# Optimization experiments

Hardware: AMD Instinct MI355X
Metric: run time of the kernel (lower is better)

The kernel has to match this reference:

```python
import jax, jax.numpy as jnp
import numpy as np

EMBED = 1024
HEADS = 16
HDIM = 64
OUT = 1024
SCALE = HDIM ** (-0.5)


def setup_inputs() -> dict:
    key = jax.random.key(0)
    ks = jax.random.split(key, 12)
    B, L = 4, 1024
    k = jax.random.normal(ks[0], (B, L, EMBED), dtype=jnp.float32)
    q = jax.random.normal(ks[1], (B, L, EMBED), dtype=jnp.float32)
    v = jax.random.normal(ks[2], (B, L, EMBED), dtype=jnp.float32)
    # Linear params stored as [in, out]; scaled like torch default init
    lim = EMBED ** (-0.5)
    Wq = jax.random.uniform(ks[3], (EMBED, HEADS * HDIM), jnp.float32, -lim, lim)
    bq = jax.random.uniform(ks[4], (HEADS * HDIM,), jnp.float32, -lim, lim)
    Wk = jax.random.uniform(ks[5], (EMBED, HEADS * HDIM), jnp.float32, -lim, lim)
    Wv = jax.random.uniform(ks[6], (EMBED, HEADS * HDIM), jnp.float32, -lim, lim)
    limp = (HEADS * HDIM) ** (-0.5)
    Wp = jax.random.uniform(ks[7], (HEADS * HDIM, OUT), jnp.float32, -limp, limp)
    bp = jax.random.uniform(ks[8], (OUT,), jnp.float32, -limp, limp)
    attn_w = jax.random.uniform(ks[9], (2 * HDIM,), jnp.float32, -SCALE, SCALE)
    gamma = jnp.ones((OUT,), jnp.float32)
    beta = jnp.zeros((OUT,), jnp.float32)
    return {"k": k, "q": q, "v": v, "Wq": Wq, "bq": bq, "Wk": Wk, "Wv": Wv,
            "Wp": Wp, "bp": bp, "attn_w": attn_w, "gamma": gamma, "beta": beta}


def reference(k, q, v, Wq, bq, Wk, Wv, Wp, bp, attn_w, gamma, beta):
    B, Lq = q.shape[0], q.shape[1]
    Lk = k.shape[1]
    # QKV projections -> (b, len, heads, hdim)
    qh = (q @ Wq + bq).reshape(B, Lq, HEADS, HDIM)
    kh = (k @ Wk).reshape(B, Lk, HEADS, HDIM)
    vh = (v @ Wv).reshape(B, Lk, HEADS, HDIM)
    # mlp score: tanh(cat(q_i, k_j) . w) == tanh(q_i.w1 + k_j.w2); avoids
    # materializing the (b, q, k, n, 2d) padded tensor from the original.
    w1, w2 = attn_w[:HDIM], attn_w[HDIM:]
    sq = jnp.einsum('bind,d->bin', qh, w1)  # (b, q_len, heads)
    sk = jnp.einsum('bjnd,d->bjn', kh, w2)  # (b, k_len, heads)
    attn = jnp.tanh(sq[:, :, None, :] + sk[:, None, :, :])  # (b, i, j, n)
    attn = jax.nn.softmax(attn, axis=2)  # softmax over k_len (dim=2)
    out = jnp.einsum('bijn,bjnd->bind', attn, vh).reshape(B, Lq, HEADS * HDIM)
    out = out @ Wp + bp
    # LayerNorm eps=1e-6 (dropout is identity at p=0)
    mean = jnp.mean(out, axis=-1, keepdims=True)
    var = jnp.var(out, axis=-1, keepdims=True)
    out = (out - mean) / jnp.sqrt(var + 1e-6) * gamma + beta
    return out
```

## Files before the change

kernel.cpp:

```cpp
#include <hip/hip_runtime.h>
#include <math.h>

#define SEQ   1024
#define EMB   1024
#define MN    16

typedef _Float16 f16;
typedef __attribute__((ext_vector_type(4))) _Float16 f16x4;
typedef __attribute__((ext_vector_type(8))) _Float16 f16x8;
typedef __attribute__((ext_vector_type(4))) float f32x4;

__global__ __launch_bounds__(256) void prep_kernel(
    const float* __restrict__ Wq, const float* __restrict__ Wk,
    const float* __restrict__ bq, const float* __restrict__ aw,
    const float* __restrict__ v, const float* __restrict__ Wv,
    float* __restrict__ uq, float* __restrict__ uk,
    float* __restrict__ cq, float* __restrict__ Wn,
    f16* __restrict__ vTh, f16* __restrict__ WvTh)
{
  __shared__ float tile[64][65];
  const int t = blockIdx.x, tid = threadIdx.x;
  if (t < 128) {
    int idx = t*256 + tid;
    bool isQ = idx < 16384;
    int li = isQ ? idx : idx - 16384;
    int e = li >> 4, n = li & 15;
    const float* W = isQ ? Wq : Wk;
    const float* w = isQ ? aw : aw + 64;
    const float* wp = &W[(size_t)e*EMB + n*64];
    float s = 0.f;
    #pragma unroll 16
    for (int d = 0; d < 64; ++d) s = fmaf(wp[d], w[d], s);
    (isQ ? uq : uk)[li] = s;
  } else if (t < 1408) {
    int tt = t - 128;
    int z = tt >> 8;
    int ty = (tt >> 4) & 15, tx = tt & 15;
    int r0 = ty*64, c0 = tx*64;
    const float* src = (z < 4) ? &v[(size_t)(z*SEQ + r0)*EMB + c0]
                               : &Wv[(size_t)r0*EMB + c0];
    int rr = tid >> 4, c4 = (tid & 15)*4;
    #pragma unroll
    for (int i = 0; i < 4; ++i) {
      int row = rr + i*16;
      float4 wv = *reinterpret_cast<const float4*>(&src[(size_t)row*EMB + c4]);
      tile[row][c4] = wv.x; tile[row][c4+1] = wv.y;
      tile[row][c4+2] = wv.z; tile[row][c4+3] = wv.w;
    }
    __syncthreads();
    #pragma unroll
    for (int i = 0; i < 4; ++i) {
      int cc = rr + i*16;
      f16x4 hh;
      #pragma unroll
      for (int jj = 0; jj < 4; ++jj) hh[jj] = (f16)tile[c4+jj][cc];
      size_t o = (z < 4) ? ((size_t)(z*EMB + c0 + cc))*SEQ + r0 + c4
                         : ((size_t)(c0 + cc))*EMB + r0 + c4;
      *reinterpret_cast<f16x4*>(&((z < 4) ? vTh : WvTh)[o]) = hh;
    }
  } else if (t == 1408) {
    if (tid < 16) {
      float s = 0.f;
      for (int d = 0; d < 64; ++d) s = fmaf(bq[tid*64+d], aw[d], s);
      cq[tid] = s;
    }
  } else {
    for (int u = tid; u < 1024; u += 256) Wn[u] = 0.f;
  }
}

__global__ __launch_bounds__(256) void sqsk2_kernel(
    const float* __restrict__ q, const float* __restrict__ k,
    const float* __restrict__ uq, const float* __restrict__ uk,
    const float* __restrict__ cq, float* __restrict__ sq, float* __restrict__ sk)
{
  __shared__ float rowbuf[8][EMB];
  __shared__ float part[16][8][17];
  int bid = blockIdx.x;
  bool isQ = bid < 512;
  int row0 = (isQ ? bid : bid - 512)*8;
  const float* X = isQ ? q : k;
  const float* U = isQ ? uq : uk;
  int tid = threadIdx.x;
  #pragma unroll
  for (int p = 0; p < 8; ++p) {
    int fi = p*256 + tid;
    int r = fi >> 8, c4 = (fi & 255)*4;
    *reinterpret_cast<float4*>(&rowbuf[r][c4]) =
        *reinterpret_cast<const float4*>(&X[(size_t)(row0+r)*EMB + c4]);
  }
  __syncthreads();
  int n = tid & 15, ch = tid >> 4;
  float acc[8] = {0,0,0,0,0,0,0,0};
  #pragma unroll 4
  for (int e0 = 0; e0 < 64; ++e0) {
    int e = ch*64 + e0;
    float u = U[e*16 + n];
    #pragma unroll
    for (int r = 0; r < 8; ++r) acc[r] = fmaf(rowbuf[r][e], u, acc[r]);
  }
  #pragma unroll
  for (int r = 0; r < 8; ++r) part[ch][r][n] = acc[r];
  __syncthreads();
  if (tid < 128) {
    int r = tid >> 4, nn = tid & 15;
    float s = isQ ? cq[nn] : 0.f;
    #pragma unroll
    for (int c = 0; c < 16; ++c) s += part[c][r][nn];
    (isQ ? sq : sk)[(size_t)(row0+r)*16 + nn] = s;
  }
}

__global__ __launch_bounds__(256) void wmatn_kernel(
    const float* __restrict__ sq, const float* __restrict__ sk,
    f16* __restrict__ wh, float* __restrict__ nodes, float* __restrict__ Wn)
{
  __shared__ float smn[256], smx[256];
  __shared__ float nodesh[MN], Wnl[MN];
  const int qd = blockIdx.x, n = blockIdx.y, b = blockIdx.z;
  const int tid = threadIdx.x;
  float mn = 1e30f, mx = -1e30f;
  #pragma unroll
  for (int s = 0; s < 4; ++s) {
    float vv = sq[((size_t)(b*SEQ + tid + s*256))*16 + n];
    mn = fminf(mn, vv); mx = fmaxf(mx, vv);
  }
  smn[tid] = mn; smx[tid] = mx;
  __syncthreads();
  for (int off = 128; off > 0; off >>= 1) {
    if (tid < off) { smn[tid] = fminf(smn[tid], smn[tid+off]);
                     smx[tid] = fmaxf(smx[tid], smx[tid+off]); }
    __syncthreads();
  }
  if (tid < MN) {
    float c = 0.5f*(smn[0]+smx[0]);
    float r = fmaxf(0.5f*(smx[0]-smn[0]), 1e-4f);
    float nv = c + r*cosf(tid*(3.14159265358979323f/(MN-1)));
    nodesh[tid] = nv;
    Wnl[tid] = 0.f;
    if (qd == 0) nodes[(b*16+n)*MN + tid] = nv;
  }
  __syncthreads();
  const int j = qd*256 + tid;
  const float skv = sk[((size_t)(b*SEQ + j))*16 + n];
  const int lane = tid & 63;
  #pragma unroll 4
  for (int m = 0; m < MN; ++m) {
    float s = nodesh[m] + skv;
    float e2 = __expf(2.f*s);
    float th = 1.f - 2.f/(e2+1.f);
    float w = __expf(th);
    wh[(size_t)(b*256 + n*MN + m)*1024 + j] = (f16)w;
    float ws = w;
    #pragma unroll
    for (int off = 32; off > 0; off >>= 1) ws += __shfl_xor(ws, off);
    if (lane == 0) atomicAdd(&Wnl[m], ws);
  }
  __syncthreads();
  if (tid < MN) atomicAdd(&Wn[(b*16+n)*MN + tid], Wnl[tid]);
}

__global__ __launch_bounds__(256) void g1c_kernel(
    const f16* __restrict__ wh, const f16* __restrict__ vTh,
    f16* __restrict__ Ph,
    const float* __restrict__ sq, const float* __restrict__ nodes,
    const float* __restrict__ Wn, f16* __restrict__ csh, f16* __restrict__ csl)
{
  __shared__ __align__(16) char SMEM[16384];
  const int t = blockIdx.x, tid = threadIdx.x;
  if (t < 256) {
    int swz = (t & 7)*32 + (t >> 3);
    int bx = swz & 15, by = swz >> 4;
    int z = by >> 2;
    int grow = by*64, bcol = bx*64;
    int wid = tid >> 6, lane = tid & 63;
    int wm = wid >> 1, wn = wid & 1;
    int asel = lane >> 4, l15 = lane & 15;
    const f16* Bz = vTh + (size_t)z*EMB*SEQ;
    char* lds = SMEM;
    f32x4 acc[2][2];
    #pragma unroll
    for (int i = 0; i < 2; ++i)
      #pragma unroll
      for (int jx = 0; jx < 2; ++jx)
        acc[i][jx] = (f32x4){0.f,0.f,0.f,0.f};
    for (int kt = 0; kt < 16; ++kt) {
      const int k0 = kt*64;
      __syncthreads();
      #pragma unroll
      for (int r = 0; r < 4; ++r) {
        int ci = ((r & 1) << 8) + tid;
        int row = ci >> 3, kc = ci & 7;
        int kcg = kc ^ (row & 7);
        const f16* base = (r < 2) ? wh : Bz;
        size_t roff = (r < 2) ? (size_t)(grow + row) : (size_t)(bcol + row);
        const char* src = (const char*)(base + roff*1024 + k0 + kcg*8);
        char* dst = lds + (r*256 + wid*64)*16;
        __builtin_amdgcn_global_load_lds(
            (const __attribute__((address_space(1))) unsigned int*)src,
            (__attribute__((address_space(3))) unsigned int*)dst, 16, 0, 0);
      }
      __syncthreads();
      #pragma unroll
      for (int kk = 0; kk < 2; ++kk) {
        f16x8 afh[2], bfh[2];
        #pragma unroll
        for (int mf = 0; mf < 2; ++mf) {
          int row = wm*32 + mf*16 + l15;
          int kcx = (kk*4 + asel) ^ (row & 7);
          afh[mf] = *reinterpret_cast<const f16x8*>(lds + row*128 + kcx*16);
        }
        #pragma unroll
        for (int nf = 0; nf < 2; ++nf) {
          int col = wn*32 + nf*16 + l15;
          int kcx = (kk*4 + asel) ^ (col & 7);
          bfh[nf] = *reinterpret_cast<const f16x8*>(lds + 8192 + col*128 + kcx*16);
        }
        #pragma unroll
        for (int mf = 0; mf < 2; ++mf)
          #pragma unroll
          for (int nf = 0; nf < 2; ++nf)
            acc[mf][nf] = __builtin_amdgcn_mfma_f32_16x16x32_f16(afh[mf], bfh[nf], acc[mf][nf], 0, 0, 0);
      }
    }
    const int crow0 = grow + wm*32 + asel*4;
    const int ccol0 = bcol + wn*32 + l15;
    #pragma unroll
    for (int nf = 0; nf < 2; ++nf)
      #pragma unroll
      for (int mf = 0; mf < 2; ++mf)
        #pragma unroll
        for (int jx = 0; jx < 4; ++jx)
          Ph[(size_t)(crow0 + mf*16 + jx)*1024 + ccol0 + nf*16] = (f16)acc[mf][nf][jx];
  } else {
    int tc = t - 256;
    int ic = tc & 63, b = tc >> 6;
    float (*nsh)[MN] = (float(*)[MN])SMEM;
    float (*wsh)[MN] = ((float(*)[MN])SMEM) + 16;
    {
      int nn = tid >> 4, mm = tid & 15;
      nsh[nn][mm] = nodes[(b*16+nn)*MN + mm];
      wsh[nn][mm] = Wn[(b*16+nn)*MN + mm];
    }
    __syncthreads();
    int il = tid >> 4, n = tid & 15;
    int i = ic*16 + il;
    float s = sq[((size_t)(b*SEQ + i))*16 + n];
    float lam[MN];
    float den = 0.f;
    int ex = -1;
    #pragma unroll
    for (int m = 0; m < MN; ++m) {
      float diff = s - nsh[n][m];
      float wb = ((m == 0) | (m == MN-1)) ? 0.5f : 1.0f;
      wb = (m & 1) ? -wb : wb;
      if (diff == 0.f) ex = m;
      lam[m] = wb / diff;
      den = fmaf(lam[m], wsh[n][m], den);
    }
    float rden = 1024.f / den;
    f16* hp = &csh[((size_t)(b*SEQ + i))*256 + n*MN];
    f16* lp = &csl[((size_t)(b*SEQ + i))*256 + n*MN];
    #pragma unroll
    for (int m8 = 0; m8 < 2; ++m8) {
      f16x8 hv, lv;
      #pragma unroll
      for (int jj = 0; jj < 8; ++jj) {
        int m = m8*8 + jj;
        float c = (ex >= 0) ? ((m == ex) ? 1024.f/wsh[n][ex] : 0.f) : lam[m]*rden;
        f16 h = (f16)c;
        hv[jj] = h; lv[jj] = (f16)(c - (float)h);
      }
      *reinterpret_cast<f16x8*>(&hp[m8*8]) = hv;
      *reinterpret_cast<f16x8*>(&lp[m8*8]) = lv;
    }
  }
}

__global__ __launch_bounds__(256) void ghprep_kernel(
    const f16* __restrict__ Ph, const f16* __restrict__ WvTh,
    const float* __restrict__ Wp, f16* __restrict__ Hsh, f16* __restrict__ Hsl)
{
  __shared__ float Gsh[MN][64];
  const int oc = blockIdx.x, n = blockIdx.y, b = blockIdx.z;
  const int bn = b*16 + n;
  const int tid = threadIdx.x;
  const int w = tid >> 6, lane = tid & 63;
  const int l15 = lane & 15, asel = lane >> 4;
  f32x4 acc = (f32x4){0.f,0.f,0.f,0.f};
  #pragma unroll 4
  for (int ks = 0; ks < 32; ++ks) {
    size_t bo = ((size_t)(n*64 + w*16 + l15))*1024 + ks*32 + asel*8;
    f16x8 bh = *reinterpret_cast<const f16x8*>(&WvTh[bo]);
    size_t ao = ((size_t)(bn*MN + l15))*1024 + ks*32 + asel*8;
    f16x8 ah = *reinterpret_cast<const f16x8*>(&Ph[ao]);
    acc = __builtin_amdgcn_mfma_f32_16x16x32_f16(ah, bh, acc, 0, 0, 0);
  }
  #pragma unroll
  for (int jx = 0; jx < 4; ++jx)
    Gsh[asel*4 + jx][w*16 + l15] = acc[jx];
  __syncthreads();
  const int o = oc*256 + tid;
  float a2[MN];
  #pragma unroll
  for (int m = 0; m < MN; ++m) a2[m] = 0.f;
  for (int d = 0; d < 64; ++d) {
    float wp = Wp[(size_t)(n*64 + d)*1024 + o];
    #pragma unroll
    for (int m = 0; m < MN; ++m) a2[m] = fmaf(wp, Gsh[m][d], a2[m]);
  }
  f16 hbuf[MN], lbuf[MN];
  #pragma unroll
  for (int m = 0; m < MN; ++m) {
    float vv = a2[m] * (1.f/1024.f);
    f16 h = (f16)vv;
    hbuf[m] = h; lbuf[m] = (f16)(vv - (float)h);
  }
  size_t base = ((size_t)(b*1024 + o))*256 + n*MN;
  #pragma unroll
  for (int m8 = 0; m8 < 2; ++m8) {
    *reinterpret_cast<f16x8*>(&Hsh[base + m8*8]) = *reinterpret_cast<f16x8*>(&hbuf[m8*8]);
    *reinterpret_cast<f16x8*>(&Hsl[base + m8*8]) = *reinterpret_cast<f16x8*>(&lbuf[m8*8]);
  }
}

__global__ __launch_bounds__(256) void gemm2_k(
    const f16* __restrict__ Ah, const f16* __restrict__ Al,
    const f16* __restrict__ Bh, const f16* __restrict__ Bl,
    const float* __restrict__ bias, float* __restrict__ Cf)
{
  __shared__ __align__(16) char lds[49152];
  const int tid = threadIdx.x;
  const int wid = tid >> 6, lane = tid & 63;
  int flat = (blockIdx.z * 8 + blockIdx.y) * 16 + blockIdx.x;
  int swz = (flat & 7) * 64 + (flat >> 3);
  const int bx = swz & 15;
  const int t2 = swz >> 4;
  const int by = t2 & 7, z = t2 >> 3;
  const int brow = by * 128;
  const int bcol = bx * 64;
  const int wm = wid >> 1, wn = wid & 1;
  const int asel = lane >> 4, l15 = lane & 15;
  const int K = 256, N = 1024, MZ = 1024;
  const f16* Az_h = Ah + (size_t)z*MZ*K;
  const f16* Az_l = Al + (size_t)z*MZ*K;
  const f16* Bz_h = Bh + (size_t)z*N*K;
  const f16* Bz_l = Bl + (size_t)z*N*K;

  f32x4 acc[4][2];
  #pragma unroll
  for (int i = 0; i < 4; ++i)
    #pragma unroll
    for (int jx = 0; jx < 2; ++jx)
      acc[i][jx] = (f32x4){0.f, 0.f, 0.f, 0.f};

  for (int t = 0; t < 4; ++t) {
    const int k0 = t * 64;
    __syncthreads();
    #pragma unroll
    for (int r = 0; r < 12; ++r) {
      const char* src;
      if (r < 8) {
        int ci = ((r & 3) << 8) + tid;
        int row = ci >> 3, kc = ci & 7;
        int kcg = kc ^ (row & 7);
        const f16* base = (r < 4) ? Az_h : Az_l;
        src = (const char*)(base + (size_t)(brow + row) * K + k0 + kcg * 8);
      } else {
        int ci = ((r & 1) << 8) + tid;
        int col = ci >> 3, kc = ci & 7;
        int kcg = kc ^ (col & 7);
        const f16* base = (r < 10) ? Bz_h : Bz_l;
        src = (const char*)(base + (size_t)(bcol + col) * K + k0 + kcg * 8);
      }
      char* dst = lds + (r * 256 + wid * 64) * 16;
      __builtin_amdgcn_global_load_lds(
          (const __attribute__((address_space(1))) unsigned int*)src,
          (__attribute__((address_space(3))) unsigned int*)dst, 16, 0, 0);
    }
    __syncthreads();
    #pragma unroll
    for (int kk = 0; kk < 2; ++kk) {
      f16x8 afh[4], afl[4], bfh[2], bfl[2];
      #pragma unroll
      for (int mf = 0; mf < 4; ++mf) {
        int row = wm * 64 + mf * 16 + l15;
        int kcx = (kk * 4 + asel) ^ (row & 7);
        int off = row * 128 + kcx * 16;
        afh[mf] = *reinterpret_cast<const f16x8*>(lds + off);
        afl[mf] = *reinterpret_cast<const f16x8*>(lds + 16384 + off);
      }
      #pragma unroll
      for (int nf = 0; nf < 2; ++nf) {
        int col = wn * 32 + nf * 16 + l15;
        int kcx = (kk * 4 + asel) ^ (col & 7);
        int off = col * 128 + kcx * 16;
        bfh[nf] = *reinterpret_cast<const f16x8*>(lds + 32768 + off);
        bfl[nf] = *reinterpret_cast<const f16x8*>(lds + 40960 + off);
      }
      #pragma unroll
      for (int mf = 0; mf < 4; ++mf)
        #pragma unroll
        for (int nf = 0; nf < 2; ++nf) {
          acc[mf][nf] = __builtin_amdgcn_mfma_f32_16x16x32_f16(afh[mf], bfh[nf], acc[mf][nf], 0, 0, 0);
          acc[mf][nf] = __builtin_amdgcn_mfma_f32_16x16x32_f16(afh[mf], bfl[nf], acc[mf][nf], 0, 0, 0);
          acc[mf][nf] = __builtin_amdgcn_mfma_f32_16x16x32_f16(afl[mf], bfh[nf], acc[mf][nf], 0, 0, 0);
        }
    }
  }
  const int crow0 = z*MZ + brow + wm * 64 + asel * 4;
  const int ccol0 = bcol + wn * 32 + l15;
  #pragma unroll
  for (int nf = 0; nf < 2; ++nf) {
    float bv = bias[ccol0 + nf * 16];
    #pragma unroll
    for (int mf = 0; mf < 4; ++mf)
      #pragma unroll
      for (int jx = 0; jx < 4; ++jx)
        Cf[(size_t)(crow0 + mf*16 + jx) * N + ccol0 + nf*16] = acc[mf][nf][jx] + bv;
  }
}

__global__ __launch_bounds__(256) void ln_kernel(
    float* __restrict__ out, const float* __restrict__ gamma,
    const float* __restrict__ beta)
{
  const int t = blockIdx.x, tid = threadIdx.x;
  int wid = tid >> 6, lane = tid & 63;
  int row = t*4 + wid;
  float4 x[4];
  float sum = 0.f, ssq = 0.f;
  #pragma unroll
  for (int p = 0; p < 4; ++p) {
    x[p] = *reinterpret_cast<float4*>(&out[(size_t)row*1024 + (p*64 + lane)*4]);
    sum += x[p].x + x[p].y + x[p].z + x[p].w;
    ssq += x[p].x*x[p].x + x[p].y*x[p].y + x[p].z*x[p].z + x[p].w*x[p].w;
  }
  #pragma unroll
  for (int off = 32; off > 0; off >>= 1) {
    sum += __shfl_xor(sum, off);
    ssq += __shfl_xor(ssq, off);
  }
  float mean = sum * (1.f/1024.f);
  float var  = ssq * (1.f/1024.f) - mean*mean;
  float inv  = 1.0f / sqrtf(var + 1e-6f);
  #pragma unroll
  for (int p = 0; p < 4; ++p) {
    float4 gv = *reinterpret_cast<const float4*>(&gamma[(p*64 + lane)*4]);
    float4 bv = *reinterpret_cast<const float4*>(&beta[(p*64 + lane)*4]);
    float4 y;
    y.x = (x[p].x - mean)*inv*gv.x + bv.x;
    y.y = (x[p].y - mean)*inv*gv.y + bv.y;
    y.z = (x[p].z - mean)*inv*gv.z + bv.z;
    y.w = (x[p].w - mean)*inv*gv.w + bv.w;
    *reinterpret_cast<float4*>(&out[(size_t)row*1024 + (p*64 + lane)*4]) = y;
  }
}

extern "C" void kernel_launch(void* const* d_in, const int* in_sizes, int n_in,
                              void* d_out, int out_size, void* d_ws, size_t ws_size,
                              hipStream_t stream)
{
  const float* k   = (const float*)d_in[0];
  const float* q   = (const float*)d_in[1];
  const float* v   = (const float*)d_in[2];
  const float* Wq  = (const float*)d_in[3];
  const float* bq  = (const float*)d_in[4];
  const float* Wk  = (const float*)d_in[5];
  const float* Wv  = (const float*)d_in[6];
  const float* Wp  = (const float*)d_in[7];
  const float* bp  = (const float*)d_in[8];
  const float* aw  = (const float*)d_in[9];
  const float* gamma = (const float*)d_in[10];
  const float* beta  = (const float*)d_in[11];
  float* out = (float*)d_out;

  float* ws    = (float*)d_ws;
  float* uq    = ws;
  float* uk    = uq + 16384;
  float* cq    = uk + 16384;
  float* sq    = cq + 16;
  float* sk    = sq + 65536;
  float* nodes = sk + 65536;
  float* Wn    = nodes + 1024;
  const size_t MEG = 1048576;
  f16* f16b = (f16*)(ws + 165904);
  f16* WvTh = f16b;
  f16* vTh  = f16b + 1*MEG;
  f16* wh   = f16b + 5*MEG;
  f16* Ph   = f16b + 6*MEG;
  f16* csh  = f16b + 7*MEG;
  f16* csl  = f16b + 8*MEG;
  f16* Hsh  = f16b + 9*MEG;
  f16* Hsl  = f16b + 10*MEG;

  prep_kernel<<<1410, 256, 0, stream>>>(Wq, Wk, bq, aw, v, Wv,
                                        uq, uk, cq, Wn, vTh, WvTh);
  sqsk2_kernel<<<1024, 256, 0, stream>>>(q, k, uq, uk, cq, sq, sk);
  wmatn_kernel<<<dim3(4,16,4), 256, 0, stream>>>(sq, sk, wh, nodes, Wn);
  g1c_kernel<<<512, 256, 0, stream>>>(wh, vTh, Ph, sq, nodes, Wn, csh, csl);
  ghprep_kernel<<<dim3(4,16,4), 256, 0, stream>>>(Ph, WvTh, Wp, Hsh, Hsl);
  gemm2_k<<<dim3(16,8,4), 256, 0, stream>>>(csh, csl, Hsh, Hsl, bp, out);
  ln_kernel<<<1024, 256, 0, stream>>>(out, gamma, beta);
}
```

Measured before the change: 183.2 us.

## Cache transposed fp16 score vectors in registers and vectorize weight-matrix writes

The prep kernel now writes the per-head score projection vectors transposed and in fp16, so each sqsk2 thread can load its 64 coefficients into registers once. The 32 KB shared-memory row staging and its barrier are dropped, and q/k rows are read straight from global with float4 loads. wmatn now computes four consecutive keys per thread and stores them as one f16x4 write instead of scalar fp16 stores. The risks are fp16 rounding of the projection coefficients and higher register pressure from the 64-float array.

After: 198.4 us. +8.3%, slower.

```diff
diff --git a/kernel.cpp b/kernel.cpp
--- a/kernel.cpp
+++ b/kernel.cpp
@@ -14,7 +14,7 @@
     const float* __restrict__ Wq, const float* __restrict__ Wk,
     const float* __restrict__ bq, const float* __restrict__ aw,
     const float* __restrict__ v, const float* __restrict__ Wv,
-    float* __restrict__ uq, float* __restrict__ uk,
+    f16* __restrict__ uqT, f16* __restrict__ ukT,
     float* __restrict__ cq, float* __restrict__ Wn,
     f16* __restrict__ vTh, f16* __restrict__ WvTh)
 {
@@ -31,7 +31,7 @@
     float s = 0.f;
     #pragma unroll 16
     for (int d = 0; d < 64; ++d) s = fmaf(wp[d], w[d], s);
-    (isQ ? uq : uk)[li] = s;
+    (isQ ? uqT : ukT)[n*1024 + e] = (f16)s;
   } else if (t < 1408) {
     int tt = t - 128;
     int z = tt >> 8;
@@ -71,33 +71,36 @@
 
 __global__ __launch_bounds__(256) void sqsk2_kernel(
     const float* __restrict__ q, const float* __restrict__ k,
-    const float* __restrict__ uq, const float* __restrict__ uk,
+    const f16* __restrict__ uqT, const f16* __restrict__ ukT,
     const float* __restrict__ cq, float* __restrict__ sq, float* __restrict__ sk)
 {
-  __shared__ float rowbuf[8][EMB];
   __shared__ float part[16][8][17];
   int bid = blockIdx.x;
   bool isQ = bid < 512;
   int row0 = (isQ ? bid : bid - 512)*8;
   const float* X = isQ ? q : k;
-  const float* U = isQ ? uq : uk;
+  const f16* U = isQ ? uqT : ukT;
   int tid = threadIdx.x;
-  #pragma unroll
-  for (int p = 0; p < 8; ++p) {
-    int fi = p*256 + tid;
-    int r = fi >> 8, c4 = (fi & 255)*4;
-    *reinterpret_cast<float4*>(&rowbuf[r][c4]) =
-        *reinterpret_cast<const float4*>(&X[(size_t)(row0+r)*EMB + c4]);
-  }
-  __syncthreads();
   int n = tid & 15, ch = tid >> 4;
+  float uf[64];
+  #pragma unroll
+  for (int qd = 0; qd < 16; ++qd) {
+    f16x4 uv = *reinterpret_cast<const f16x4*>(&U[n*1024 + ch*64 + qd*4]);
+    uf[qd*4+0] = (float)uv[0]; uf[qd*4+1] = (float)uv[1];
+    uf[qd*4+2] = (float)uv[2]; uf[qd*4+3] = (float)uv[3];
+  }
   float acc[8] = {0,0,0,0,0,0,0,0};
-  #pragma unroll 4
-  for (int e0 = 0; e0 < 64; ++e0) {
-    int e = ch*64 + e0;
-    float u = U[e*16 + n];
-    #pragma unroll
-    for (int r = 0; r < 8; ++r) acc[r] = fmaf(rowbuf[r][e], u, acc[r]);
+  #pragma unroll
+  for (int r = 0; r < 8; ++r) {
+    const float* Xr = &X[(size_t)(row0+r)*EMB + ch*64];
+    #pragma unroll
+    for (int qd = 0; qd < 16; ++qd) {
+      float4 a = *reinterpret_cast<const float4*>(&Xr[qd*4]);
+      acc[r] = fmaf(a.x, uf[qd*4+0], acc[r]);
+      acc[r] = fmaf(a.y, uf[qd*4+1], acc[r]);
+      acc[r] = fmaf(a.z, uf[qd*4+2], acc[r]);
+      acc[r] = fmaf(a.w, uf[qd*4+3], acc[r]);
+    }
   }
   #pragma unroll
   for (int r = 0; r < 8; ++r) part[ch][r][n] = acc[r];
@@ -141,20 +144,31 @@
     if (qd == 0) nodes[(b*16+n)*MN + tid] = nv;
   }
   __syncthreads();
-  const int j = qd*256 + tid;
-  const float skv = sk[((size_t)(b*SEQ + j))*16 + n];
-  const int lane = tid & 63;
-  #pragma unroll 4
-  for (int m = 0; m < MN; ++m) {
-    float s = nodesh[m] + skv;
-    float e2 = __expf(2.f*s);
-    float th = 1.f - 2.f/(e2+1.f);
-    float w = __expf(th);
-    wh[(size_t)(b*256 + n*MN + m)*1024 + j] = (f16)w;
-    float ws = w;
-    #pragma unroll
-    for (int off = 32; off > 0; off >>= 1) ws += __shfl_xor(ws, off);
-    if (lane == 0) atomicAdd(&Wnl[m], ws);
+  const int jq = tid & 63, mg = tid >> 6;
+  const int j0 = qd*256 + jq*4;
+  float skv[4];
+  #pragma unroll
+  for (int jj = 0; jj < 4; ++jj)
+    skv[jj] = sk[((size_t)(b*SEQ + j0 + jj))*16 + n];
+  #pragma unroll
+  for (int mm = 0; mm < 4; ++mm) {
+    int m = mg*4 + mm;
+    float nm = nodesh[m];
+    f16x4 hv;
+    float wsum = 0.f;
+    #pragma unroll
+    for (int jj = 0; jj < 4; ++jj) {
+      float s = nm + skv[jj];
+      float e2 = __expf(2.f*s);
+      float th = 1.f - 2.f/(e2+1.f);
+      float w = __expf(th);
+      hv[jj] = (f16)w;
+      wsum += w;
+    }
+    *reinterpret_cast<f16x4*>(&wh[(size_t)(b*256 + n*MN + m)*1024 + j0]) = hv;
+    #pragma unroll
+    for (int off = 32; off > 0; off >>= 1) wsum += __shfl_xor(wsum, off);
+    if (jq == 0) atomicAdd(&Wnl[m], wsum);
   }
   __syncthreads();
   if (tid < MN) atomicAdd(&Wn[(b*16+n)*MN + tid], Wnl[tid]);
@@ -476,27 +490,27 @@
   float* out = (float*)d_out;
 
   float* ws    = (float*)d_ws;
-  float* uq    = ws;
-  float* uk    = uq + 16384;
-  float* cq    = uk + 16384;
+  float* cq    = ws;
   float* sq    = cq + 16;
   float* sk    = sq + 65536;
   float* nodes = sk + 65536;
   float* Wn    = nodes + 1024;
   const size_t MEG = 1048576;
-  f16* f16b = (f16*)(ws + 165904);
-  f16* WvTh = f16b;
-  f16* vTh  = f16b + 1*MEG;
-  f16* wh   = f16b + 5*MEG;
-  f16* Ph   = f16b + 6*MEG;
-  f16* csh  = f16b + 7*MEG;
-  f16* csl  = f16b + 8*MEG;
-  f16* Hsh  = f16b + 9*MEG;
-  f16* Hsl  = f16b + 10*MEG;
+  f16* f16b = (f16*)(ws + 133136);
+  f16* uqT  = f16b;
+  f16* ukT  = f16b + 16384;
+  f16* WvTh = f16b + 32768;
+  f16* vTh  = WvTh + MEG;
+  f16* wh   = vTh + 4*MEG;
+  f16* Ph   = wh + MEG;
+  f16* csh  = Ph + MEG;
+  f16* csl  = csh + MEG;
+  f16* Hsh  = csl + MEG;
+  f16* Hsl  = Hsh + MEG;
 
   prep_kernel<<<1410, 256, 0, stream>>>(Wq, Wk, bq, aw, v, Wv,
-                                        uq, uk, cq, Wn, vTh, WvTh);
-  sqsk2_kernel<<<1024, 256, 0, stream>>>(q, k, uq, uk, cq, sq, sk);
+                                        uqT, ukT, cq, Wn, vTh, WvTh);
+  sqsk2_kernel<<<1024, 256, 0, stream>>>(q, k, uqT, ukT, cq, sq, sk);
   wmatn_kernel<<<dim3(4,16,4), 256, 0, stream>>>(sq, sk, wh, nodes, Wn);
   g1c_kernel<<<512, 256, 0, stream>>>(wh, vTh, Ph, sq, nodes, Wn, csh, csl);
   ghprep_kernel<<<dim3(4,16,4), 256, 0, stream>>>(Ph, WvTh, Wp, Hsh, Hsl);
```
